# Performance work log

Hardware: AMD Instinct MI355X
Metric: run time of the kernel (lower is better)

Reference implementation:

```python
import jax, jax.numpy as jnp
import numpy as np
from itertools import combinations

NUM_FIELDS = 40
EMB_DIM = 64
BATCH = 2048
PAIRS = NUM_FIELDS * (NUM_FIELDS - 1) // 2  # 780

def _triu_indices():
    idx = np.array(list(combinations(range(NUM_FIELDS), 2)), dtype=np.int32)  # [PAIRS, 2]
    return idx[:, 0], idx[:, 1]

def setup_inputs() -> dict:
    key = jax.random.key(0)
    k1, k2 = jax.random.split(key)
    feature_emb = jax.random.normal(k1, (BATCH, NUM_FIELDS, EMB_DIM), dtype=jnp.float32)
    # xavier_normal for [PAIRS, EMB_DIM, EMB_DIM]: fan_in = fan_out = EMB_DIM
    std = float(np.sqrt(2.0 / (EMB_DIM + EMB_DIM)))
    bilinear_W = jax.random.normal(k2, (PAIRS, EMB_DIM, EMB_DIM), dtype=jnp.float32) * std
    left_idx, right_idx = _triu_indices()
    return {
        "feature_emb": feature_emb,
        "bilinear_W": bilinear_W,
        "left_idx": jnp.asarray(left_idx),
        "right_idx": jnp.asarray(right_idx),
    }

def reference(feature_emb, bilinear_W, left_idx, right_idx):
    # field_interaction: per-pair bilinear form
    left_emb = feature_emb[:, left_idx]    # [B, PAIRS, D]
    right_emb = feature_emb[:, right_idx]  # [B, PAIRS, D]
    # (left @ W_p) * right, per pair p
    out = jnp.einsum('bpd,pde->bpe', left_emb, bilinear_W) * right_emb
    return out
```

## Files before the change

kernel.cpp:

```cpp
#include <hip/hip_runtime.h>

#define BATCH   2048
#define NFIELDS 40
#define EMB     64
#define PAIRS   780
#define BM      128
#define NTILES  (BATCH / BM)
#define NBLOCKS (PAIRS * NTILES)

typedef __attribute__((ext_vector_type(8))) short          short8;
typedef __attribute__((ext_vector_type(8))) unsigned short ushort8;
typedef __attribute__((ext_vector_type(4))) float          fvec4;

__device__ __forceinline__ unsigned short f2bf(float f) {
    unsigned int x = __float_as_uint(f);
    return (unsigned short)((x + 0x7fffu + ((x >> 16) & 1u)) >> 16);
}
__device__ __forceinline__ float bf2f(unsigned short h) {
    return __uint_as_float(((unsigned int)h) << 16);
}

__global__ __launch_bounds__(256, 2) void bilinear_kernel(
    const float* __restrict__ femb, const float* __restrict__ W,
    const int* __restrict__ lidx, const int* __restrict__ ridx,
    float* __restrict__ out)
{
    __shared__ unsigned short Wh[64 * 64];
    __shared__ unsigned short Wl[64 * 64];
    __shared__ unsigned short Lh[BM * 64];
    __shared__ unsigned short Ll[BM * 64];

    int d   = blockIdx.x;
    int w   = (d & 7) * (NBLOCKS / 8) + (d >> 3);
    int p   = w >> 4;
    int b0  = (w & 15) * BM;

    int lp = lidx[p];
    int rp = ridx[p];
    int t  = threadIdx.x;

    {
        const float* Wp = W + (size_t)p * (EMB * EMB);
        int e  = t & 63;
        int k0 = (t >> 6) * 16;
        #pragma unroll
        for (int c2 = 0; c2 < 2; ++c2) {
            ushort8 hi, lo;
            int kb = k0 + c2 * 8;
            #pragma unroll
            for (int i = 0; i < 8; ++i) {
                float f = Wp[(size_t)(kb + i) * EMB + e];
                unsigned short h = f2bf(f);
                hi[i] = h;
                lo[i] = f2bf(f - bf2f(h));
            }
            int chunk = kb >> 3;
            int dst   = e * 64 + ((chunk ^ (e & 7)) << 3);
            *(ushort8*)&Wh[dst] = hi;
            *(ushort8*)&Wl[dst] = lo;
        }
    }
    {
        int row = t >> 1;
        int k0  = (t & 1) * 32;
        const float* Lr = femb + ((size_t)(b0 + row) * NFIELDS + lp) * EMB + k0;
        #pragma unroll
        for (int c2 = 0; c2 < 4; ++c2) {
            fvec4 fa = *(const fvec4*)&Lr[c2 * 8];
            fvec4 fb = *(const fvec4*)&Lr[c2 * 8 + 4];
            ushort8 hi, lo;
            #pragma unroll
            for (int i = 0; i < 4; ++i) {
                unsigned short h = f2bf(fa[i]);
                hi[i] = h; lo[i] = f2bf(fa[i] - bf2f(h));
                unsigned short h2 = f2bf(fb[i]);
                hi[i + 4] = h2; lo[i + 4] = f2bf(fb[i] - bf2f(h2));
            }
            int chunk = (k0 >> 3) + c2;
            int dst   = row * 64 + ((chunk ^ (row & 7)) << 3);
            *(ushort8*)&Lh[dst] = hi;
            *(ushort8*)&Ll[dst] = lo;
        }
    }
    __syncthreads();

    int wv   = t >> 6;
    int l    = t & 63;
    int lrow = l & 15;
    int lgrp = l >> 4;

    fvec4 acc[2][4] = {};
    #pragma unroll
    for (int kk = 0; kk < 2; ++kk) {
        int kbase = kk * 32 + lgrp * 8;
        int chunk = kbase >> 3;
        short8 Ah[2], Al[2];
        #pragma unroll
        for (int m = 0; m < 2; ++m) {
            int r   = wv * 32 + m * 16 + lrow;
            int src = r * 64 + ((chunk ^ (r & 7)) << 3);
            Ah[m] = *(short8*)&Lh[src];
            Al[m] = *(short8*)&Ll[src];
        }
        #pragma unroll
        for (int n = 0; n < 4; ++n) {
            int e   = n * 16 + lrow;
            int src = e * 64 + ((chunk ^ (e & 7)) << 3);
            short8 Bh = *(short8*)&Wh[src];
            short8 Bl = *(short8*)&Wl[src];
            #pragma unroll
            for (int m = 0; m < 2; ++m) {
                acc[m][n] = __builtin_amdgcn_mfma_f32_16x16x32_bf16(Al[m], Bh, acc[m][n], 0, 0, 0);
                acc[m][n] = __builtin_amdgcn_mfma_f32_16x16x32_bf16(Ah[m], Bl, acc[m][n], 0, 0, 0);
                acc[m][n] = __builtin_amdgcn_mfma_f32_16x16x32_bf16(Ah[m], Bh, acc[m][n], 0, 0, 0);
            }
        }
    }

    #pragma unroll
    for (int m = 0; m < 2; ++m) {
        int rb = b0 + wv * 32 + m * 16 + lgrp * 4;
        #pragma unroll
        for (int r = 0; r < 4; ++r) {
            int b = rb + r;
            const float* Rr = femb + ((size_t)b * NFIELDS + rp) * EMB;
            float*       Or = out  + ((size_t)b * PAIRS   + p)  * EMB;
            #pragma unroll
            for (int n = 0; n < 4; ++n) {
                int col = n * 16 + lrow;
                Or[col] = acc[m][n][r] * Rr[col];
            }
        }
    }
}

extern "C" void kernel_launch(void* const* d_in, const int* in_sizes, int n_in,
                              void* d_out, int out_size, void* d_ws, size_t ws_size,
                              hipStream_t stream) {
    const float* femb = (const float*)d_in[0];
    const float* W    = (const float*)d_in[1];
    const int*   lidx = (const int*)d_in[2];
    const int*   ridx = (const int*)d_in[3];
    float*       out  = (float*)d_out;
    bilinear_kernel<<<NBLOCKS, 256, 0, stream>>>(femb, W, lidx, ridx, out);
}
```

Before: 521.9 us.

## Precompute bf16 hi/lo splits in prep kernels and load MFMA operands from global

Adds two prep kernels that split feature embeddings and W into bf16 hi/lo halves in workspace once, instead of redoing the split per block. The main kernel drops shared memory and loads MFMA operands straight from global. Operand roles are swapped (W becomes A, features become B) so each lane holds four contiguous output columns, which allows vectorized float4 loads of the right embedding and float4 stores. Occupancy hint is raised to 4. The cost is extra launches and workspace traffic, plus uncoalesced-ish global operand loads that now lean on cache.

```diff
diff --git a/kernel.cpp b/kernel.cpp
--- a/kernel.cpp
+++ b/kernel.cpp
@@ -7,6 +7,8 @@
 #define BM      128
 #define NTILES  (BATCH / BM)
 #define NBLOCKS (PAIRS * NTILES)
+#define FEMB_ELEMS (BATCH * NFIELDS * EMB)
+#define W_ELEMS    (PAIRS * EMB * EMB)
 
 typedef __attribute__((ext_vector_type(8))) short          short8;
 typedef __attribute__((ext_vector_type(8))) unsigned short ushort8;
@@ -19,117 +21,125 @@
 __device__ __forceinline__ float bf2f(unsigned short h) {
     return __uint_as_float(((unsigned int)h) << 16);
 }
+struct bfpair { unsigned short h, l; };
+__device__ __forceinline__ bfpair split1(float f) {
+    bfpair r;
+    r.h = f2bf(f);
+    r.l = f2bf(f - bf2f(r.h));
+    return r;
+}
 
-__global__ __launch_bounds__(256, 2) void bilinear_kernel(
-    const float* __restrict__ femb, const float* __restrict__ W,
+__global__ __launch_bounds__(256) void prep_femb(
+    const float* __restrict__ femb, unsigned short* __restrict__ Fh,
+    unsigned short* __restrict__ Fl)
+{
+    int tid  = blockIdx.x * 256 + threadIdx.x;
+    int base = tid * 8;
+    fvec4 a = *(const fvec4*)&femb[base];
+    fvec4 b = *(const fvec4*)&femb[base + 4];
+    ushort8 hi, lo;
+    #pragma unroll
+    for (int i = 0; i < 4; ++i) {
+        bfpair s0 = split1(a[i]);
+        hi[i] = s0.h; lo[i] = s0.l;
+        bfpair s1 = split1(b[i]);
+        hi[i + 4] = s1.h; lo[i + 4] = s1.l;
+    }
+    *(ushort8*)&Fh[base] = hi;
+    *(ushort8*)&Fl[base] = lo;
+}
+
+__global__ __launch_bounds__(256) void prep_w(
+    const float* __restrict__ W, unsigned short* __restrict__ Wh,
+    unsigned short* __restrict__ Wl)
+{
+    __shared__ float Ws[EMB * EMB];
+    int p = blockIdx.x;
+    int t = threadIdx.x;
+    const float* Wp = W + (size_t)p * (EMB * EMB);
+    #pragma unroll
+    for (int j = 0; j < 4; ++j)
+        *(fvec4*)&Ws[t * 16 + j * 4] = *(const fvec4*)&Wp[t * 16 + j * 4];
+    __syncthreads();
+
+    int e  = t & 63;
+    int k0 = (t >> 6) * 16;
+    #pragma unroll
+    for (int j = 0; j < 2; ++j) {
+        int k = k0 + j * 8;
+        ushort8 hi, lo;
+        #pragma unroll
+        for (int i = 0; i < 8; ++i) {
+            bfpair s = split1(Ws[(k + i) * EMB + e]);
+            hi[i] = s.h; lo[i] = s.l;
+        }
+        size_t dst = (size_t)p * (EMB * EMB) + e * EMB + k;
+        *(ushort8*)&Wh[dst] = hi;
+        *(ushort8*)&Wl[dst] = lo;
+    }
+}
+
+__global__ __launch_bounds__(256, 4) void bilinear_main(
+    const unsigned short* __restrict__ Fh, const unsigned short* __restrict__ Fl,
+    const unsigned short* __restrict__ Wh, const unsigned short* __restrict__ Wl,
+    const float* __restrict__ femb,
     const int* __restrict__ lidx, const int* __restrict__ ridx,
     float* __restrict__ out)
 {
-    __shared__ unsigned short Wh[64 * 64];
-    __shared__ unsigned short Wl[64 * 64];
-    __shared__ unsigned short Lh[BM * 64];
-    __shared__ unsigned short Ll[BM * 64];
-
-    int d   = blockIdx.x;
-    int w   = (d & 7) * (NBLOCKS / 8) + (d >> 3);
-    int p   = w >> 4;
-    int b0  = (w & 15) * BM;
+    int d  = blockIdx.x;
+    int w  = (d & 7) * (NBLOCKS / 8) + (d >> 3);
+    int p  = w >> 4;
+    int b0 = (w & 15) * BM;
 
     int lp = lidx[p];
     int rp = ridx[p];
     int t  = threadIdx.x;
+    int wv = t >> 6;
+    int l  = t & 63;
+    int r  = l & 15;
+    int g  = l >> 4;
 
-    {
-        const float* Wp = W + (size_t)p * (EMB * EMB);
-        int e  = t & 63;
-        int k0 = (t >> 6) * 16;
-        #pragma unroll
-        for (int c2 = 0; c2 < 2; ++c2) {
-            ushort8 hi, lo;
-            int kb = k0 + c2 * 8;
-            #pragma unroll
-            for (int i = 0; i < 8; ++i) {
-                float f = Wp[(size_t)(kb + i) * EMB + e];
-                unsigned short h = f2bf(f);
-                hi[i] = h;
-                lo[i] = f2bf(f - bf2f(h));
-            }
-            int chunk = kb >> 3;
-            int dst   = e * 64 + ((chunk ^ (e & 7)) << 3);
-            *(ushort8*)&Wh[dst] = hi;
-            *(ushort8*)&Wl[dst] = lo;
-        }
-    }
-    {
-        int row = t >> 1;
-        int k0  = (t & 1) * 32;
-        const float* Lr = femb + ((size_t)(b0 + row) * NFIELDS + lp) * EMB + k0;
-        #pragma unroll
-        for (int c2 = 0; c2 < 4; ++c2) {
-            fvec4 fa = *(const fvec4*)&Lr[c2 * 8];
-            fvec4 fb = *(const fvec4*)&Lr[c2 * 8 + 4];
-            ushort8 hi, lo;
-            #pragma unroll
-            for (int i = 0; i < 4; ++i) {
-                unsigned short h = f2bf(fa[i]);
-                hi[i] = h; lo[i] = f2bf(fa[i] - bf2f(h));
-                unsigned short h2 = f2bf(fb[i]);
-                hi[i + 4] = h2; lo[i + 4] = f2bf(fb[i] - bf2f(h2));
-            }
-            int chunk = (k0 >> 3) + c2;
-            int dst   = row * 64 + ((chunk ^ (row & 7)) << 3);
-            *(ushort8*)&Lh[dst] = hi;
-            *(ushort8*)&Ll[dst] = lo;
-        }
-    }
-    __syncthreads();
-
-    int wv   = t >> 6;
-    int l    = t & 63;
-    int lrow = l & 15;
-    int lgrp = l >> 4;
+    const unsigned short* WhP = Wh + (size_t)p * (EMB * EMB);
+    const unsigned short* WlP = Wl + (size_t)p * (EMB * EMB);
 
     fvec4 acc[2][4] = {};
     #pragma unroll
     for (int kk = 0; kk < 2; ++kk) {
-        int kbase = kk * 32 + lgrp * 8;
-        int chunk = kbase >> 3;
-        short8 Ah[2], Al[2];
+        short8 Ah[4], Al[4], Bh[2], Bl[2];
+        #pragma unroll
+        for (int n = 0; n < 4; ++n) {
+            int off = (n * 16 + r) * EMB + kk * 32 + g * 8;
+            Ah[n] = *(const short8*)&WhP[off];
+            Al[n] = *(const short8*)&WlP[off];
+        }
         #pragma unroll
         for (int m = 0; m < 2; ++m) {
-            int r   = wv * 32 + m * 16 + lrow;
-            int src = r * 64 + ((chunk ^ (r & 7)) << 3);
-            Ah[m] = *(short8*)&Lh[src];
-            Al[m] = *(short8*)&Ll[src];
+            size_t off = ((size_t)(b0 + wv * 32 + m * 16 + r) * NFIELDS + lp) * EMB
+                       + kk * 32 + g * 8;
+            Bh[m] = *(const short8*)&Fh[off];
+            Bl[m] = *(const short8*)&Fl[off];
         }
         #pragma unroll
-        for (int n = 0; n < 4; ++n) {
-            int e   = n * 16 + lrow;
-            int src = e * 64 + ((chunk ^ (e & 7)) << 3);
-            short8 Bh = *(short8*)&Wh[src];
-            short8 Bl = *(short8*)&Wl[src];
+        for (int m = 0; m < 2; ++m)
             #pragma unroll
-            for (int m = 0; m < 2; ++m) {
-                acc[m][n] = __builtin_amdgcn_mfma_f32_16x16x32_bf16(Al[m], Bh, acc[m][n], 0, 0, 0);
-                acc[m][n] = __builtin_amdgcn_mfma_f32_16x16x32_bf16(Ah[m], Bl, acc[m][n], 0, 0, 0);
-                acc[m][n] = __builtin_amdgcn_mfma_f32_16x16x32_bf16(Ah[m], Bh, acc[m][n], 0, 0, 0);
+            for (int n = 0; n < 4; ++n) {
+                acc[m][n] = __builtin_amdgcn_mfma_f32_16x16x32_bf16(Al[n], Bh[m], acc[m][n], 0, 0, 0);
+                acc[m][n] = __builtin_amdgcn_mfma_f32_16x16x32_bf16(Ah[n], Bl[m], acc[m][n], 0, 0, 0);
+                acc[m][n] = __builtin_amdgcn_mfma_f32_16x16x32_bf16(Ah[n], Bh[m], acc[m][n], 0, 0, 0);
             }
-        }
     }
 
     #pragma unroll
     for (int m = 0; m < 2; ++m) {
-        int rb = b0 + wv * 32 + m * 16 + lgrp * 4;
+        int b = b0 + wv * 32 + m * 16 + r;
+        const float* Rr = femb + ((size_t)b * NFIELDS + rp) * EMB;
+        float*       Or = out  + ((size_t)b * PAIRS   + p)  * EMB;
         #pragma unroll
-        for (int r = 0; r < 4; ++r) {
-            int b = rb + r;
-            const float* Rr = femb + ((size_t)b * NFIELDS + rp) * EMB;
-            float*       Or = out  + ((size_t)b * PAIRS   + p)  * EMB;
-            #pragma unroll
-            for (int n = 0; n < 4; ++n) {
-                int col = n * 16 + lrow;
-                Or[col] = acc[m][n][r] * Rr[col];
-            }
+        for (int n = 0; n < 4; ++n) {
+            int e0 = n * 16 + g * 4;
+            fvec4 rv = *(const fvec4*)&Rr[e0];
+            fvec4 o  = acc[m][n] * rv;
+            *(fvec4*)&Or[e0] = o;
         }
     }
 }
@@ -142,5 +152,13 @@
     const int*   lidx = (const int*)d_in[2];
     const int*   ridx = (const int*)d_in[3];
     float*       out  = (float*)d_out;
-    bilinear_kernel<<<NBLOCKS, 256, 0, stream>>>(femb, W, lidx, ridx, out);
+
+    unsigned short* Fh  = (unsigned short*)d_ws;
+    unsigned short* Fl  = Fh + FEMB_ELEMS;
+    unsigned short* Whg = Fl + FEMB_ELEMS;
+    unsigned short* Wlg = Whg + W_ELEMS;
+
+    prep_femb<<<FEMB_ELEMS / (256 * 8), 256, 0, stream>>>(femb, Fh, Fl);
+    prep_w   <<<PAIRS, 256, 0, stream>>>(W, Whg, Wlg);
+    bilinear_main<<<NBLOCKS, 256, 0, stream>>>(Fh, Fl, Whg, Wlg, femb, lidx, ridx, out);
 }
```

Measured after the change: 591.0 us. +13.3%, slower.
